# Kernel optimization log

Measured on AMD Instinct MI355X. Metric: run time of the kernel, lower is better.

## Reference

```python
import jax, jax.numpy as jnp
import numpy as np

V = 100000      # num nodes
E = 600000      # num edges (even: first half in-edges, second half out-edges)
D_IN = 128
D_OUT = 128
NREL2 = 100     # num_rel * 2
BN_EPS = 1e-5


def ccorr(a, b):
    # circular correlation along last dim: irfft(conj(rfft(a)) * rfft(b), n=d)
    d = a.shape[-1]
    return jnp.fft.irfft(jnp.conj(jnp.fft.rfft(a)) * jnp.fft.rfft(b), n=d).astype(a.dtype)


def setup_inputs() -> dict:
    key = jax.random.key(0)
    ks = jax.random.split(key, 12)
    return {
        "x": jax.random.normal(ks[0], (V, D_IN), dtype=jnp.float32),
        "rel_repr": jax.random.normal(ks[1], (NREL2, D_IN), dtype=jnp.float32),
        "edge_norm": jax.random.uniform(ks[2], (E,), dtype=jnp.float32),
        "in_w": jax.random.normal(ks[3], (D_IN, D_OUT), dtype=jnp.float32) * 0.05,
        "out_w": jax.random.normal(ks[4], (D_IN, D_OUT), dtype=jnp.float32) * 0.05,
        "loop_w": jax.random.normal(ks[5], (D_IN, D_OUT), dtype=jnp.float32) * 0.05,
        "w_rel": jax.random.normal(ks[6], (D_IN, D_OUT), dtype=jnp.float32) * 0.05,
        "loop_rel": jax.random.normal(ks[7], (1, D_IN), dtype=jnp.float32),
        "bias": jnp.zeros((D_OUT,), dtype=jnp.float32),
        "bn_gamma": jnp.ones((D_OUT,), dtype=jnp.float32),
        "bn_beta": jnp.zeros((D_OUT,), dtype=jnp.float32),
        "edge_src": jax.random.randint(ks[8], (E,), 0, V, dtype=jnp.int32),
        "edge_dst": jax.random.randint(ks[9], (E,), 0, V, dtype=jnp.int32),
        "edge_type": jax.random.randint(ks[10], (E,), 0, NREL2, dtype=jnp.int32),
    }


def reference(x, rel_repr, edge_norm, in_w, out_w, loop_w, w_rel, loop_rel,
              bias, bn_gamma, bn_beta, edge_src, edge_dst, edge_type):
    rel = rel_repr  # rel_wt is None (num_base=-1)
    # gather src features per edge and compose with relation embedding (corr)
    edge_data = ccorr(x[edge_src], rel[edge_type])             # [E, D_IN]
    half = edge_data.shape[0] // 2
    msg = jnp.concatenate(
        [edge_data[:half] @ in_w, edge_data[half:] @ out_w], axis=0
    ) * edge_norm[:, None]                                     # [E, D_OUT]
    # scatter-sum into destination nodes
    agg = jax.ops.segment_sum(msg, edge_dst, num_segments=V)   # [V, D_OUT]
    # self-loop term
    loop = ccorr(x, jnp.broadcast_to(loop_rel, x.shape)) @ loop_w
    h = (agg + loop) / 3.0 + bias
    # BatchNorm1d (training mode: batch stats, biased variance)
    mean = h.mean(axis=0)
    var = h.var(axis=0)
    h = (h - mean) * jax.lax.rsqrt(var + BN_EPS) * bn_gamma + bn_beta
    # act is identity; ltr=True -> project relations
    return h, rel @ w_rel
```

## Files before the change

kernel.cpp:

```cpp
#include <hip/hip_runtime.h>
#include <hip/hip_bf16.h>

#define D 128
constexpr int V_N    = 100000;
constexpr int E_N    = 600000;
constexpr int HALF_E = E_N / 2;
constexpr int NREL2  = 100;
constexpr int NBUCK  = 2 * NREL2;
constexpr float BN_EPS_F = 1e-5f;

constexpr int CHUNK  = 4096;
constexpr int NCHUNK = (E_N + CHUNK - 1) / CHUNK;

typedef short bf16x8  __attribute__((ext_vector_type(8)));
typedef float f32x16  __attribute__((ext_vector_type(16)));
typedef float f32x4v  __attribute__((ext_vector_type(4)));
typedef unsigned int uint32;

constexpr int LOOP_GRID2 = 782;
constexpr size_t MT_BYTES  = 201ull * D * D * 2;
constexpr size_t AGG_BYTES = (size_t)V_N * D * 2;

constexpr size_t P_SS_OFF  = MT_BYTES;
constexpr size_t P_SD_OFF  = P_SS_OFF + (size_t)E_N * 4;
constexpr size_t P_SN_OFF  = P_SD_OFF + (size_t)E_N * 4;
constexpr size_t P_AGG_OFF = P_SN_OFF + (size_t)E_N * 4;
constexpr size_t P_HIST_OFF = P_AGG_OFF;
constexpr size_t P_COFF_OFF = P_HIST_OFF + (size_t)NBUCK * NCHUNK * 4;
constexpr size_t P_CS_OFF  = P_AGG_OFF + AGG_BYTES;
constexpr size_t P_CQ_OFF  = P_CS_OFF + 512;
constexpr size_t P_CNT_OFF = P_CQ_OFF + 512;
constexpr size_t P_ST_OFF  = P_CNT_OFF + 1024;
constexpr size_t WS_NEED_PK = P_ST_OFF + 1024;
constexpr size_t P2_XBF  = (WS_NEED_PK + 255) & ~(size_t)255;
constexpr size_t P2_PSUM = P2_XBF + AGG_BYTES;
constexpr size_t P2_PSQ  = P2_PSUM + 128ull * LOOP_GRID2 * 4;
constexpr size_t WS_NEED2 = P2_PSQ + 128ull * LOOP_GRID2 * 4;

constexpr size_t V4_SS   = MT_BYTES;
constexpr size_t V4_SD   = V4_SS + (size_t)E_N * 4;
constexpr size_t V4_SN   = V4_SD + (size_t)E_N * 4;
constexpr size_t V4_XBF  = V4_SN + (size_t)E_N * 4;
constexpr size_t V4_AGG  = V4_XBF + AGG_BYTES;
constexpr size_t V4_DEG  = V4_AGG + AGG_BYTES;
constexpr size_t V4_CS   = V4_DEG + (size_t)V_N * 4;
constexpr size_t V4_CQ   = V4_CS + 512;
constexpr size_t V4_RP   = V4_CQ + 512;
constexpr size_t V4_CUR  = V4_RP + (size_t)(V_N + 16) * 4;
constexpr size_t V4_EIDX = V4_CUR + (size_t)V_N * 4;
constexpr size_t V4_HIST = V4_EIDX + (size_t)E_N * 4;
constexpr size_t V4_COFF = V4_HIST + (size_t)NBUCK * NCHUNK * 4;
constexpr size_t V4_CNT  = V4_COFF + (size_t)NBUCK * NCHUNK * 4;
constexpr size_t V4_ST   = V4_CNT + 1024;
constexpr size_t V4_BSUM = V4_ST + 1024;
constexpr size_t V4_PSUM = (V4_BSUM + 1024 + 255) & ~(size_t)255;
constexpr size_t V4_PSQ  = V4_PSUM + 128ull * LOOP_GRID2 * 4;
constexpr size_t V4_MSG  = (V4_PSQ + 128ull * LOOP_GRID2 * 4 + 255) & ~(size_t)255;
constexpr size_t WS_NEED4 = V4_MSG + (size_t)E_N * D * 2;

constexpr int SCAN_ELEMS = 1024;
constexpr int NSCANB = (V_N + SCAN_ELEMS - 1) / SCAN_ELEMS;

__device__ inline unsigned short f2bf(float f) {
    __hip_bfloat16 h = __float2bfloat16(f);
    return __builtin_bit_cast(unsigned short, h);
}
__device__ inline float bf2f(unsigned int u) {
    return __uint_as_float(u << 16);
}
__device__ inline int bucket_of(int e, const int* __restrict__ etype) {
    return etype[e] + (e < HALF_E ? 0 : NREL2);
}

__global__ __launch_bounds__(256) void k_hist_chunk(const int* __restrict__ etype,
                                                    int* __restrict__ hist) {
    __shared__ int h[NBUCK];
    for (int i = threadIdx.x; i < NBUCK; i += 256) h[i] = 0;
    __syncthreads();
    int c = blockIdx.x;
    int e0 = c * CHUNK;
#pragma unroll
    for (int r = 0; r < CHUNK / 256; r++) {
        int e = e0 + r * 256 + threadIdx.x;
        if (e < E_N) atomicAdd(&h[bucket_of(e, etype)], 1);
    }
    __syncthreads();
    for (int b = threadIdx.x; b < NBUCK; b += 256) hist[b * NCHUNK + c] = h[b];
}

__global__ void k_scan_bucket(const int* __restrict__ hist, int* __restrict__ chunkoff,
                              int* __restrict__ counts) {
    int b = blockIdx.x, lane = threadIdx.x;
    int acc = 0;
    for (int base = 0; base < NCHUNK; base += 64) {
        int c = base + lane;
        int v = (c < NCHUNK) ? hist[b * NCHUNK + c] : 0;
        int s = v;
#pragma unroll
        for (int off = 1; off < 64; off <<= 1) {
            int t = __shfl(s, lane - off, 64);
            if (lane >= off) s += t;
        }
        if (c < NCHUNK) chunkoff[b * NCHUNK + c] = acc + (s - v);
        acc += __shfl(s, 63, 64);
    }
    if (lane == 0) counts[b] = acc;
}

__global__ void k_scan(const int* __restrict__ counts, int* __restrict__ starts) {
    __shared__ int s[256];
    int i = threadIdx.x;
    int v = (i < NBUCK) ? counts[i] : 0;
    s[i] = v;
    __syncthreads();
    for (int off = 1; off < 256; off <<= 1) {
        int t = (i >= off) ? s[i - off] : 0;
        __syncthreads();
        s[i] += t;
        __syncthreads();
    }
    if (i < NBUCK) starts[i] = s[i] - v;
    if (i == 255) starts[NBUCK] = s[255];
}

__global__ __launch_bounds__(256) void k_scatter2(
    const int* __restrict__ src, const int* __restrict__ dst,
    const float* __restrict__ norm, const int* __restrict__ etype,
    const int* __restrict__ starts, const int* __restrict__ chunkoff,
    int* __restrict__ ssrc, int* __restrict__ sdst, float* __restrict__ snorm) {
    __shared__ int h[NBUCK];
    __shared__ int sbase[NBUCK];
    int c = blockIdx.x;
    for (int b = threadIdx.x; b < NBUCK; b += 256) {
        h[b] = 0;
        sbase[b] = starts[b] + chunkoff[b * NCHUNK + c];
    }
    __syncthreads();
    int e0 = c * CHUNK;
#pragma unroll
    for (int r = 0; r < CHUNK / 256; r++) {
        int e = e0 + r * 256 + threadIdx.x;
        if (e < E_N) {
            int b = bucket_of(e, etype);
            int rank = atomicAdd(&h[b], 1);
            int p = sbase[b] + rank;
            ssrc[p] = src[e]; sdst[p] = dst[e]; snorm[p] = norm[e];
        }
    }
}

constexpr int SETUP_XBF_BLOCKS = 800;
constexpr int SETUP_GRID = 201 + 50 + SETUP_XBF_BLOCKS;
__global__ void k_setup(const float* __restrict__ x, const float* __restrict__ rel,
                        const float* __restrict__ in_w, const float* __restrict__ out_w,
                        const float* __restrict__ loop_rel, const float* __restrict__ loop_w,
                        const float* __restrict__ w_rel, ushort* __restrict__ MT,
                        ushort* __restrict__ xbf, float* __restrict__ out2) {
    extern __shared__ float smem[];
    int blk = blockIdx.x;
    if (blk < 201) {
        float* sW = smem;
        float* sR = smem + D * D;
        int b = blk;
        const float* r = (b < NREL2) ? rel + (size_t)b * D
                       : (b < NBUCK) ? rel + (size_t)(b - NREL2) * D : loop_rel;
        const float* W = (b < NREL2) ? in_w : (b < NBUCK) ? out_w : loop_w;
        for (int i = threadIdx.x; i < D * D; i += blockDim.x) sW[i] = W[i];
        for (int i = threadIdx.x; i < D; i += blockDim.x) { float v = r[i]; sR[i] = v; sR[i + D] = v; }
        __syncthreads();
        int o  = threadIdx.x & 127;
        int jg = threadIdx.x >> 7;
        ushort* MTb = MT + (size_t)b * (D * D);
        for (int pass = 0; pass < 4; pass++) {
            int jbase = jg * 64 + pass * 16;
            float acc[16];
#pragma unroll
            for (int t = 0; t < 16; t++) acc[t] = 0.f;
            for (int k = 0; k < D; k++) {
                float w = sW[k * D + o];
#pragma unroll
                for (int t = 0; t < 16; t++) acc[t] += sR[jbase + t + k] * w;
            }
#pragma unroll
            for (int t = 0; t < 16; t++) MTb[(size_t)o * D + jbase + t] = f2bf(acc[t]);
        }
    } else if (blk < 251) {
        int rr = (blk - 201) * 2 + (threadIdx.x >> 7);
        int o  = threadIdx.x & 127;
        float acc = 0.f;
        for (int k = 0; k < D; k++) acc += rel[rr * D + k] * w_rel[k * D + o];
        out2[rr * D + o] = acc;
    } else {
        const int N8 = V_N * D / 8;
        for (int i = (blk - 251) * 256 + threadIdx.x; i < N8; i += SETUP_XBF_BLOCKS * 256) {
            f32x4v v0 = *(const f32x4v*)&x[(size_t)i * 8];
            f32x4v v1 = *(const f32x4v*)&x[(size_t)i * 8 + 4];
            union { ushort u[8]; uint4 q; } t;
            t.u[0] = f2bf(v0[0]); t.u[1] = f2bf(v0[1]); t.u[2] = f2bf(v0[2]); t.u[3] = f2bf(v0[3]);
            t.u[4] = f2bf(v1[0]); t.u[5] = f2bf(v1[1]); t.u[6] = f2bf(v1[2]); t.u[7] = f2bf(v1[3]);
            *(uint4*)&xbf[(size_t)i * 8] = t.q;
        }
    }
}

__global__ __launch_bounds__(256) void k_deg(const int* __restrict__ sdst,
                                             int* __restrict__ deg) {
    int p = blockIdx.x * 256 + threadIdx.x;
    if (p < E_N) atomicAdd(&deg[sdst[p]], 1);
}

__global__ __launch_bounds__(256) void k_scan1(const int* __restrict__ deg,
                                               int* __restrict__ rowptr,
                                               int* __restrict__ blocksum) {
    __shared__ int s[256];
    int blk = blockIdx.x, tid = threadIdx.x;
    int base = blk * SCAN_ELEMS + tid * 4;
    int v[4]; int tot = 0;
#pragma unroll
    for (int j = 0; j < 4; j++) { int i = base + j; v[j] = (i < V_N) ? deg[i] : 0; tot += v[j]; }
    s[tid] = tot;
    __syncthreads();
    for (int off = 1; off < 256; off <<= 1) {
        int t = (tid >= off) ? s[tid - off] : 0;
        __syncthreads();
        s[tid] += t;
        __syncthreads();
    }
    int run = s[tid] - tot;
#pragma unroll
    for (int j = 0; j < 4; j++) { int i = base + j; if (i < V_N) rowptr[i] = run; run += v[j]; }
    if (tid == 255) blocksum[blk] = s[255];
}

__global__ void k_scan2(int* __restrict__ blocksum) {
    __shared__ int s[128];
    int i = threadIdx.x;
    int v = (i < NSCANB) ? blocksum[i] : 0;
    s[i] = v;
    __syncthreads();
    for (int off = 1; off < 128; off <<= 1) {
        int t = (i >= off) ? s[i - off] : 0;
        __syncthreads();
        s[i] += t;
        __syncthreads();
    }
    if (i < NSCANB) blocksum[i] = s[i] - v;
}

__global__ __launch_bounds__(256) void k_scan3(int* __restrict__ rowptr,
                                               const int* __restrict__ blocksum,
                                               int* __restrict__ cursor) {
    int i = blockIdx.x * 256 + threadIdx.x;
    if (i < V_N) {
        int r = rowptr[i] + blocksum[i >> 10];
        rowptr[i] = r; cursor[i] = r;
    }
    if (i == 0) rowptr[V_N] = E_N;
}

__global__ __launch_bounds__(256) void k_perm(const int* __restrict__ sdst,
                                              int* __restrict__ cursor,
                                              int* __restrict__ eidx) {
    int p = blockIdx.x * 256 + threadIdx.x;
    if (p < E_N) {
        int slot = atomicAdd(&cursor[sdst[p]], 1);
        eidx[slot] = p;
    }
}

constexpr int BPB = 8;

__global__ __launch_bounds__(256) void k_edge_st(
    const ushort* __restrict__ xbf, const ushort* __restrict__ MT,
    const int* __restrict__ starts, const int* __restrict__ ssrc,
    const float* __restrict__ snorm, uint32* __restrict__ msg32) {
    int wid  = threadIdx.x >> 6, lane = threadIdx.x & 63;
    int l31  = lane & 31, l5 = lane >> 5;
    int bucket = blockIdx.x / BPB;
    int sib    = (blockIdx.x % BPB) * 2 + (wid >> 1);
    int oh     = wid & 1;
    int bstart = starts[bucket], bend = starts[bucket + 1];
    const ushort* MTb = MT + (size_t)bucket * (D * D);
    int c0 = oh * 64 + 2 * l31;
    bf16x8 B0[8], B1[8];
#pragma unroll
    for (int kc = 0; kc < 8; kc++) {
        B0[kc] = *(const bf16x8*)&MTb[(size_t)c0 * D + kc * 16 + l5 * 8];
        B1[kc] = *(const bf16x8*)&MTb[(size_t)(c0 + 1) * D + kc * 16 + l5 * 8];
    }
    for (int tbase = bstart + sib * 32; tbase < bend; tbase += BPB * 2 * 32) {
        int nv = bend - tbase; if (nv > 32) nv = 32;
        int sr = ssrc[tbase + (l31 < nv ? l31 : 0)];
        const ushort* xr = xbf + (size_t)sr * D + l5 * 8;
        bf16x8 A[8];
#pragma unroll
        for (int kc = 0; kc < 8; kc++) A[kc] = *(const bf16x8*)(xr + kc * 16);
        f32x16 C0, C1;
#pragma unroll
        for (int i = 0; i < 16; i++) { C0[i] = 0.f; C1[i] = 0.f; }
#pragma unroll
        for (int kc = 0; kc < 8; kc++) {
            C0 = __builtin_amdgcn_mfma_f32_32x32x16_bf16(A[kc], B0[kc], C0, 0, 0, 0);
            C1 = __builtin_amdgcn_mfma_f32_32x32x16_bf16(A[kc], B1[kc], C1, 0, 0, 0);
        }
#pragma unroll
        for (int r = 0; r < 16; r++) {
            int rw = (r & 3) + 8 * (r >> 2) + 4 * l5;
            if (rw < nv) {
                int p = tbase + rw;
                float nm = snorm[p];
                uint32 u = (uint32)f2bf(C0[r] * nm) | ((uint32)f2bf(C1[r] * nm) << 16);
                msg32[(size_t)p * 64 + oh * 32 + l31] = u;
            }
        }
    }
}

__global__ __launch_bounds__(256) void k_segsum(
    const uint32* __restrict__ msg32, const int* __restrict__ eidx,
    const int* __restrict__ rowptr, uint32* __restrict__ agg32) {
    int v = blockIdx.x * 4 + (threadIdx.x >> 6);
    if (v >= V_N) return;
    int lane = threadIdx.x & 63;
    int s = rowptr[v], e = rowptr[v + 1];
    float a0 = 0.f, a1 = 0.f;
    for (int i = s; i < e; i++) {
        int p = eidx[i];
        uint32 u = msg32[(size_t)p * 64 + lane];
        a0 += bf2f(u & 0xffffu); a1 += bf2f(u >> 16);
    }
    agg32[(size_t)v * 64 + lane] = (uint32)f2bf(a0) | ((uint32)f2bf(a1) << 16);
}

__global__ __launch_bounds__(256) void k_loop_pair(
    const ushort* __restrict__ xbf, const ushort* __restrict__ MT,
    const float* __restrict__ bias, const uint32* __restrict__ agg32,
    float* __restrict__ out, float* __restrict__ psum, float* __restrict__ psq) {
    __shared__ float lsum[128], lsq[128];
    if (threadIdx.x < 128) { lsum[threadIdx.x] = 0.f; lsq[threadIdx.x] = 0.f; }
    int wid = threadIdx.x >> 6, lane = threadIdx.x & 63;
    int l31 = lane & 31, l5 = lane >> 5;
    int oh  = wid & 1;
    int strm = blockIdx.x * 2 + (wid >> 1);
    const int NSTR = LOOP_GRID2 * 2;
    const ushort* MTb = MT + (size_t)NBUCK * (D * D);
    int c0 = oh * 64 + 2 * l31;
    int jj = oh * 32 + l31;
    bf16x8 B0[8], B1[8];
#pragma unroll
    for (int kc = 0; kc < 8; kc++) {
        B0[kc] = *(const bf16x8*)&MTb[(size_t)c0 * D + kc * 16 + l5 * 8];
        B1[kc] = *(const bf16x8*)&MTb[(size_t)(c0 + 1) * D + kc * 16 + l5 * 8];
    }
    float b0 = bias[c0], b1 = bias[c0 + 1];
    float ps0 = 0.f, pq0 = 0.f, ps1 = 0.f, pq1 = 0.f;
    const int NT = V_N / 32;
    for (int tile = strm; tile < NT; tile += NSTR) {
        int tbase = tile * 32;
        const ushort* xr = xbf + (size_t)(tbase + l31) * D + l5 * 8;
        bf16x8 A[8];
#pragma unroll
        for (int kc = 0; kc < 8; kc++) A[kc] = *(const bf16x8*)(xr + kc * 16);
        f32x16 C0, C1;
#pragma unroll
        for (int i = 0; i < 16; i++) { C0[i] = 0.f; C1[i] = 0.f; }
#pragma unroll
        for (int kc = 0; kc < 8; kc++) {
            C0 = __builtin_amdgcn_mfma_f32_32x32x16_bf16(A[kc], B0[kc], C0, 0, 0, 0);
            C1 = __builtin_amdgcn_mfma_f32_32x32x16_bf16(A[kc], B1[kc], C1, 0, 0, 0);
        }
#pragma unroll
        for (int r = 0; r < 16; r++) {
            int rw = (r & 3) + 8 * (r >> 2) + 4 * l5;
            int row = tbase + rw;
            uint32 u = agg32[(size_t)row * 64 + jj];
            float h0 = (bf2f(u & 0xffffu) + C0[r]) * (1.f / 3.f) + b0;
            float h1 = (bf2f(u >> 16)     + C1[r]) * (1.f / 3.f) + b1;
            float2 hv = make_float2(h0, h1);
            *(float2*)&out[(size_t)row * D + c0] = hv;
            ps0 += h0; pq0 += h0 * h0;
            ps1 += h1; pq1 += h1 * h1;
        }
    }
    __syncthreads();
    atomicAdd(&lsum[c0], ps0); atomicAdd(&lsq[c0], pq0);
    atomicAdd(&lsum[c0 + 1], ps1); atomicAdd(&lsq[c0 + 1], pq1);
    __syncthreads();
    if (threadIdx.x < 128) {
        psum[(size_t)threadIdx.x * LOOP_GRID2 + blockIdx.x] = lsum[threadIdx.x];
        psq [(size_t)threadIdx.x * LOOP_GRID2 + blockIdx.x] = lsq [threadIdx.x];
    }
}

__global__ __launch_bounds__(256) void k_colreduce(
    const float* __restrict__ psum, const float* __restrict__ psq,
    float* __restrict__ colsum, float* __restrict__ colsq) {
    __shared__ float ls[256], lq[256];
    int c = blockIdx.x, tid = threadIdx.x;
    float s = 0.f, q = 0.f;
    for (int b = tid; b < LOOP_GRID2; b += 256) {
        s += psum[(size_t)c * LOOP_GRID2 + b];
        q += psq [(size_t)c * LOOP_GRID2 + b];
    }
    ls[tid] = s; lq[tid] = q;
    __syncthreads();
    for (int off = 128; off > 0; off >>= 1) {
        if (tid < off) { ls[tid] += ls[tid + off]; lq[tid] += lq[tid + off]; }
        __syncthreads();
    }
    if (tid == 0) { colsum[c] = ls[0]; colsq[c] = lq[0]; }
}

__global__ __launch_bounds__(256) void k_edge_pkb(
    const ushort* __restrict__ xbf, const ushort* __restrict__ MT,
    const int* __restrict__ starts, const int* __restrict__ ssrc,
    const int* __restrict__ sdst, const float* __restrict__ snorm,
    ushort* __restrict__ agg) {
    int wid  = threadIdx.x >> 6, lane = threadIdx.x & 63;
    int l31  = lane & 31, l5 = lane >> 5;
    int bucket = blockIdx.x / BPB;
    int sib    = (blockIdx.x % BPB) * 2 + (wid >> 1);
    int oh     = wid & 1;
    int bstart = starts[bucket], bend = starts[bucket + 1];
    const ushort* MTb = MT + (size_t)bucket * (D * D);
    int c0 = oh * 64 + 2 * l31;
    bf16x8 B0[8], B1[8];
#pragma unroll
    for (int kc = 0; kc < 8; kc++) {
        B0[kc] = *(const bf16x8*)&MTb[(size_t)c0 * D + kc * 16 + l5 * 8];
        B1[kc] = *(const bf16x8*)&MTb[(size_t)(c0 + 1) * D + kc * 16 + l5 * 8];
    }
    for (int tbase = bstart + sib * 32; tbase < bend; tbase += BPB * 2 * 32) {
        int nv = bend - tbase; if (nv > 32) nv = 32;
        int sr = ssrc[tbase + (l31 < nv ? l31 : 0)];
        const ushort* xr = xbf + (size_t)sr * D + l5 * 8;
        bf16x8 A[8];
#pragma unroll
        for (int kc = 0; kc < 8; kc++) A[kc] = *(const bf16x8*)(xr + kc * 16);
        f32x16 C0, C1;
#pragma unroll
        for (int i = 0; i < 16; i++) { C0[i] = 0.f; C1[i] = 0.f; }
#pragma unroll
        for (int kc = 0; kc < 8; kc++) {
            C0 = __builtin_amdgcn_mfma_f32_32x32x16_bf16(A[kc], B0[kc], C0, 0, 0, 0);
            C1 = __builtin_amdgcn_mfma_f32_32x32x16_bf16(A[kc], B1[kc], C1, 0, 0, 0);
        }
#pragma unroll
        for (int r = 0; r < 16; r++) {
            int rw = (r & 3) + 8 * (r >> 2) + 4 * l5;
            if (rw < nv) {
                float nm = snorm[tbase + rw];
                int   dv = sdst[tbase + rw];
                union { ushort u[2]; unsigned int w; } p;
                p.u[0] = f2bf(C0[r] * nm);
                p.u[1] = f2bf(C1[r] * nm);
                ushort* ap = agg + (size_t)dv * D + c0;
                asm volatile("global_atomic_pk_add_bf16 %0, %1, off"
                             :: "v"(ap), "v"(p.w) : "memory");
            }
        }
    }
}

__global__ void k_bn(float* __restrict__ out, const float* __restrict__ colsum,
                     const float* __restrict__ colsq, const float* __restrict__ gamma,
                     const float* __restrict__ beta) {
    const size_t N4 = (size_t)V_N * D / 4;
    size_t stride = (size_t)gridDim.x * blockDim.x;
    for (size_t q = (size_t)blockIdx.x * blockDim.x + threadIdx.x; q < N4; q += stride) {
        int c4 = (int)(q & 31);
        float4 s  = *(const float4*)&colsum[c4 * 4];
        float4 sq = *(const float4*)&colsq[c4 * 4];
        float4 g  = *(const float4*)&gamma[c4 * 4];
        float4 be = *(const float4*)&beta[c4 * 4];
        float4 h  = *(float4*)&out[q * 4];
        const float inv = 1.f / (float)V_N;
        float m0 = s.x * inv, m1 = s.y * inv, m2 = s.z * inv, m3 = s.w * inv;
        float r0 = rsqrtf(sq.x * inv - m0 * m0 + BN_EPS_F);
        float r1 = rsqrtf(sq.y * inv - m1 * m1 + BN_EPS_F);
        float r2 = rsqrtf(sq.z * inv - m2 * m2 + BN_EPS_F);
        float r3 = rsqrtf(sq.w * inv - m3 * m3 + BN_EPS_F);
        h.x = (h.x - m0) * r0 * g.x + be.x;
        h.y = (h.y - m1) * r1 * g.y + be.y;
        h.z = (h.z - m2) * r2 * g.z + be.z;
        h.w = (h.w - m3) * r3 * g.w + be.w;
        *(float4*)&out[q * 4] = h;
    }
}

extern "C" void kernel_launch(void* const* d_in, const int* in_sizes, int n_in,
                              void* d_out, int out_size, void* d_ws, size_t ws_size,
                              hipStream_t stream) {
    const float* x        = (const float*)d_in[0];
    const float* rel      = (const float*)d_in[1];
    const float* enorm    = (const float*)d_in[2];
    const float* in_w     = (const float*)d_in[3];
    const float* out_w    = (const float*)d_in[4];
    const float* loop_w   = (const float*)d_in[5];
    const float* w_rel    = (const float*)d_in[6];
    const float* loop_rel = (const float*)d_in[7];
    const float* bias     = (const float*)d_in[8];
    const float* gamma    = (const float*)d_in[9];
    const float* beta     = (const float*)d_in[10];
    const int*   esrc     = (const int*)d_in[11];
    const int*   edst     = (const int*)d_in[12];
    const int*   etype    = (const int*)d_in[13];
    float* out = (float*)d_out;
    char*  ws  = (char*)d_ws;

    const int smem = (D * D + 256) * sizeof(float);
    const int gE = (E_N + 255) / 256;

    if (ws_size >= WS_NEED4) {
        ushort* MT     = (ushort*)(ws + 0);
        int*    ssrc   = (int*)(ws + V4_SS);
        int*    sdst   = (int*)(ws + V4_SD);
        float*  snorm  = (float*)(ws + V4_SN);
        ushort* xbf    = (ushort*)(ws + V4_XBF);
        uint32* agg32  = (uint32*)(ws + V4_AGG);
        int*    deg    = (int*)(ws + V4_DEG);
        float*  colsum = (float*)(ws + V4_CS);
        float*  colsq  = (float*)(ws + V4_CQ);
        int*    rowptr = (int*)(ws + V4_RP);
        int*    cursor = (int*)(ws + V4_CUR);
        int*    eidx   = (int*)(ws + V4_EIDX);
        int*    hist   = (int*)(ws + V4_HIST);
        int*    coff   = (int*)(ws + V4_COFF);
        int*    counts = (int*)(ws + V4_CNT);
        int*    starts = (int*)(ws + V4_ST);
        int*    bsum   = (int*)(ws + V4_BSUM);
        float*  psum   = (float*)(ws + V4_PSUM);
        float*  psq    = (float*)(ws + V4_PSQ);
        uint32* msg32  = (uint32*)(ws + V4_MSG);

        hipMemsetAsync(ws + V4_DEG, 0, (size_t)V_N * 4, stream);

        k_hist_chunk<<<NCHUNK, 256, 0, stream>>>(etype, hist);
        k_scan_bucket<<<NBUCK, 64, 0, stream>>>(hist, coff, counts);
        k_scan<<<1, 256, 0, stream>>>(counts, starts);
        k_scatter2<<<NCHUNK, 256, 0, stream>>>(esrc, edst, enorm, etype, starts, coff,
                                               ssrc, sdst, snorm);
        k_setup<<<SETUP_GRID, 256, smem, stream>>>(x, rel, in_w, out_w, loop_rel, loop_w,
                                                   w_rel, MT, xbf, out + (size_t)V_N * D);
        k_deg<<<gE, 256, 0, stream>>>(sdst, deg);
        k_scan1<<<NSCANB, 256, 0, stream>>>(deg, rowptr, bsum);
        k_scan2<<<1, 128, 0, stream>>>(bsum);
        k_scan3<<<(V_N + 255) / 256, 256, 0, stream>>>(rowptr, bsum, cursor);
        k_perm<<<gE, 256, 0, stream>>>(sdst, cursor, eidx);

        k_edge_st<<<NBUCK * BPB, 256, 0, stream>>>(xbf, MT, starts, ssrc, snorm, msg32);
        k_segsum<<<(V_N + 3) / 4, 256, 0, stream>>>(msg32, eidx, rowptr, agg32);

        k_loop_pair<<<LOOP_GRID2, 256, 0, stream>>>(xbf, MT, bias, agg32, out, psum, psq);
        k_colreduce<<<128, 256, 0, stream>>>(psum, psq, colsum, colsq);
        k_bn<<<2048, 256, 0, stream>>>(out, colsum, colsq, gamma, beta);
    } else {
        ushort* MT     = (ushort*)(ws + 0);
        int*    ssrc   = (int*)(ws + P_SS_OFF);
        int*    sdst   = (int*)(ws + P_SD_OFF);
        float*  snorm  = (float*)(ws + P_SN_OFF);
        ushort* aggbf  = (ushort*)(ws + P_AGG_OFF);
        uint32* agg32  = (uint32*)(ws + P_AGG_OFF);
        int*    hist   = (int*)(ws + P_HIST_OFF);
        int*    coff   = (int*)(ws + P_COFF_OFF);
        float*  colsum = (float*)(ws + P_CS_OFF);
        float*  colsq  = (float*)(ws + P_CQ_OFF);
        int*    counts = (int*)(ws + P_CNT_OFF);
        int*    starts = (int*)(ws + P_ST_OFF);
        ushort* xbf    = (ushort*)(ws + P2_XBF);
        float*  psum   = (float*)(ws + P2_PSUM);
        float*  psq    = (float*)(ws + P2_PSQ);

        k_hist_chunk<<<NCHUNK, 256, 0, stream>>>(etype, hist);
        k_scan_bucket<<<NBUCK, 64, 0, stream>>>(hist, coff, counts);
        k_scan<<<1, 256, 0, stream>>>(counts, starts);
        k_scatter2<<<NCHUNK, 256, 0, stream>>>(esrc, edst, enorm, etype, starts, coff,
                                               ssrc, sdst, snorm);
        hipMemsetAsync(ws + P_AGG_OFF, 0, AGG_BYTES, stream);
        k_setup<<<SETUP_GRID, 256, smem, stream>>>(x, rel, in_w, out_w, loop_rel, loop_w,
                                                   w_rel, MT, xbf, out + (size_t)V_N * D);
        k_edge_pkb<<<NBUCK * BPB, 256, 0, stream>>>(xbf, MT, starts, ssrc, sdst, snorm, aggbf);
        k_loop_pair<<<LOOP_GRID2, 256, 0, stream>>>(xbf, MT, bias, agg32, out, psum, psq);
        k_colreduce<<<128, 256, 0, stream>>>(psum, psq, colsum, colsq);
        k_bn<<<2048, 256, 0, stream>>>(out, colsum, colsq, gamma, beta);
    }
}
```

Baseline: 507.2 us.

## Fuse segment-sum into self-loop GEMM and degree count into edge scatter

Removes the separate segment-sum kernel and its bf16 aggregate buffer by gathering each node's messages directly in the self-loop MFMA kernel's epilogue, which now uses a larger grid. Degree counting moves into the bucket scatter kernel, removing a separate launch and a re-read of the sorted destinations. The edge message kernel gets more blocks per bucket. The fused epilogue runs per-row CSR loops of varying length inside an MFMA wave, which can cause divergence and less regular memory access than the dedicated segment-sum kernel.

```diff
diff --git a/kernel.cpp b/kernel.cpp
--- a/kernel.cpp
+++ b/kernel.cpp
@@ -17,10 +17,10 @@
 typedef float f32x4v  __attribute__((ext_vector_type(4)));
 typedef unsigned int uint32;
 
-constexpr int LOOP_GRID2 = 782;
 constexpr size_t MT_BYTES  = 201ull * D * D * 2;
 constexpr size_t AGG_BYTES = (size_t)V_N * D * 2;
 
+constexpr int LOOP_GRID2 = 782;
 constexpr size_t P_SS_OFF  = MT_BYTES;
 constexpr size_t P_SD_OFF  = P_SS_OFF + (size_t)E_N * 4;
 constexpr size_t P_SN_OFF  = P_SD_OFF + (size_t)E_N * 4;
@@ -37,26 +37,26 @@
 constexpr size_t P2_PSQ  = P2_PSUM + 128ull * LOOP_GRID2 * 4;
 constexpr size_t WS_NEED2 = P2_PSQ + 128ull * LOOP_GRID2 * 4;
 
-constexpr size_t V4_SS   = MT_BYTES;
-constexpr size_t V4_SD   = V4_SS + (size_t)E_N * 4;
-constexpr size_t V4_SN   = V4_SD + (size_t)E_N * 4;
-constexpr size_t V4_XBF  = V4_SN + (size_t)E_N * 4;
-constexpr size_t V4_AGG  = V4_XBF + AGG_BYTES;
-constexpr size_t V4_DEG  = V4_AGG + AGG_BYTES;
-constexpr size_t V4_CS   = V4_DEG + (size_t)V_N * 4;
-constexpr size_t V4_CQ   = V4_CS + 512;
-constexpr size_t V4_RP   = V4_CQ + 512;
-constexpr size_t V4_CUR  = V4_RP + (size_t)(V_N + 16) * 4;
-constexpr size_t V4_EIDX = V4_CUR + (size_t)V_N * 4;
-constexpr size_t V4_HIST = V4_EIDX + (size_t)E_N * 4;
-constexpr size_t V4_COFF = V4_HIST + (size_t)NBUCK * NCHUNK * 4;
-constexpr size_t V4_CNT  = V4_COFF + (size_t)NBUCK * NCHUNK * 4;
-constexpr size_t V4_ST   = V4_CNT + 1024;
-constexpr size_t V4_BSUM = V4_ST + 1024;
-constexpr size_t V4_PSUM = (V4_BSUM + 1024 + 255) & ~(size_t)255;
-constexpr size_t V4_PSQ  = V4_PSUM + 128ull * LOOP_GRID2 * 4;
-constexpr size_t V4_MSG  = (V4_PSQ + 128ull * LOOP_GRID2 * 4 + 255) & ~(size_t)255;
-constexpr size_t WS_NEED4 = V4_MSG + (size_t)E_N * D * 2;
+constexpr int LOOP_GRID3 = 1563;
+constexpr size_t V5_SS   = MT_BYTES;
+constexpr size_t V5_SD   = V5_SS + (size_t)E_N * 4;
+constexpr size_t V5_SN   = V5_SD + (size_t)E_N * 4;
+constexpr size_t V5_XBF  = V5_SN + (size_t)E_N * 4;
+constexpr size_t V5_DEG  = V5_XBF + AGG_BYTES;
+constexpr size_t V5_CS   = V5_DEG + (size_t)V_N * 4;
+constexpr size_t V5_CQ   = V5_CS + 512;
+constexpr size_t V5_RP   = V5_CQ + 512;
+constexpr size_t V5_CUR  = V5_RP + (size_t)(V_N + 16) * 4;
+constexpr size_t V5_EIDX = V5_CUR + (size_t)V_N * 4;
+constexpr size_t V5_HIST = V5_EIDX + (size_t)E_N * 4;
+constexpr size_t V5_COFF = V5_HIST + (size_t)NBUCK * NCHUNK * 4;
+constexpr size_t V5_CNT  = V5_COFF + (size_t)NBUCK * NCHUNK * 4;
+constexpr size_t V5_ST   = V5_CNT + 1024;
+constexpr size_t V5_BSUM = V5_ST + 1024;
+constexpr size_t V5_PSUM = (V5_BSUM + 1024 + 255) & ~(size_t)255;
+constexpr size_t V5_PSQ  = V5_PSUM + 128ull * LOOP_GRID3 * 4;
+constexpr size_t V5_MSG  = (V5_PSQ + 128ull * LOOP_GRID3 * 4 + 255) & ~(size_t)255;
+constexpr size_t WS_NEED5 = V5_MSG + (size_t)E_N * D * 2;
 
 constexpr int SCAN_ELEMS = 1024;
 constexpr int NSCANB = (V_N + SCAN_ELEMS - 1) / SCAN_ELEMS;
@@ -123,11 +123,12 @@
     if (i == 255) starts[NBUCK] = s[255];
 }
 
-__global__ __launch_bounds__(256) void k_scatter2(
+__global__ __launch_bounds__(256) void k_scatter3(
     const int* __restrict__ src, const int* __restrict__ dst,
     const float* __restrict__ norm, const int* __restrict__ etype,
     const int* __restrict__ starts, const int* __restrict__ chunkoff,
-    int* __restrict__ ssrc, int* __restrict__ sdst, float* __restrict__ snorm) {
+    int* __restrict__ ssrc, int* __restrict__ sdst, float* __restrict__ snorm,
+    int* __restrict__ deg) {
     __shared__ int h[NBUCK];
     __shared__ int sbase[NBUCK];
     int c = blockIdx.x;
@@ -142,9 +143,11 @@
         int e = e0 + r * 256 + threadIdx.x;
         if (e < E_N) {
             int b = bucket_of(e, etype);
+            int dv = dst[e];
             int rank = atomicAdd(&h[b], 1);
             int p = sbase[b] + rank;
-            ssrc[p] = src[e]; sdst[p] = dst[e]; snorm[p] = norm[e];
+            ssrc[p] = src[e]; sdst[p] = dv; snorm[p] = norm[e];
+            atomicAdd(&deg[dv], 1);
         }
     }
 }
@@ -203,12 +206,6 @@
     }
 }
 
-__global__ __launch_bounds__(256) void k_deg(const int* __restrict__ sdst,
-                                             int* __restrict__ deg) {
-    int p = blockIdx.x * 256 + threadIdx.x;
-    if (p < E_N) atomicAdd(&deg[sdst[p]], 1);
-}
-
 __global__ __launch_bounds__(256) void k_scan1(const int* __restrict__ deg,
                                                int* __restrict__ rowptr,
                                                int* __restrict__ blocksum) {
@@ -268,12 +265,170 @@
     }
 }
 
-constexpr int BPB = 8;
-
+constexpr int EBPB = 16;
 __global__ __launch_bounds__(256) void k_edge_st(
     const ushort* __restrict__ xbf, const ushort* __restrict__ MT,
     const int* __restrict__ starts, const int* __restrict__ ssrc,
     const float* __restrict__ snorm, uint32* __restrict__ msg32) {
+    int wid  = threadIdx.x >> 6, lane = threadIdx.x & 63;
+    int l31  = lane & 31, l5 = lane >> 5;
+    int bucket = blockIdx.x / EBPB;
+    int sib    = (blockIdx.x % EBPB) * 2 + (wid >> 1);
+    int oh     = wid & 1;
+    int bstart = starts[bucket], bend = starts[bucket + 1];
+    const ushort* MTb = MT + (size_t)bucket * (D * D);
+    int c0 = oh * 64 + 2 * l31;
+    bf16x8 B0[8], B1[8];
+#pragma unroll
+    for (int kc = 0; kc < 8; kc++) {
+        B0[kc] = *(const bf16x8*)&MTb[(size_t)c0 * D + kc * 16 + l5 * 8];
+        B1[kc] = *(const bf16x8*)&MTb[(size_t)(c0 + 1) * D + kc * 16 + l5 * 8];
+    }
+    for (int tbase = bstart + sib * 32; tbase < bend; tbase += EBPB * 2 * 32) {
+        int nv = bend - tbase; if (nv > 32) nv = 32;
+        int sr = ssrc[tbase + (l31 < nv ? l31 : 0)];
+        const ushort* xr = xbf + (size_t)sr * D + l5 * 8;
+        bf16x8 A[8];
+#pragma unroll
+        for (int kc = 0; kc < 8; kc++) A[kc] = *(const bf16x8*)(xr + kc * 16);
+        f32x16 C0, C1;
+#pragma unroll
+        for (int i = 0; i < 16; i++) { C0[i] = 0.f; C1[i] = 0.f; }
+#pragma unroll
+        for (int kc = 0; kc < 8; kc++) {
+            C0 = __builtin_amdgcn_mfma_f32_32x32x16_bf16(A[kc], B0[kc], C0, 0, 0, 0);
+            C1 = __builtin_amdgcn_mfma_f32_32x32x16_bf16(A[kc], B1[kc], C1, 0, 0, 0);
+        }
+#pragma unroll
+        for (int r = 0; r < 16; r++) {
+            int rw = (r & 3) + 8 * (r >> 2) + 4 * l5;
+            if (rw < nv) {
+                int p = tbase + rw;
+                float nm = snorm[p];
+                uint32 u = (uint32)f2bf(C0[r] * nm) | ((uint32)f2bf(C1[r] * nm) << 16);
+                msg32[(size_t)p * 64 + oh * 32 + l31] = u;
+            }
+        }
+    }
+}
+
+__global__ __launch_bounds__(256) void k_loop_fused(
+    const ushort* __restrict__ xbf, const ushort* __restrict__ MT,
+    const float* __restrict__ bias, const uint32* __restrict__ msg32,
+    const int* __restrict__ eidx, const int* __restrict__ rowptr,
+    float* __restrict__ out, float* __restrict__ psum, float* __restrict__ psq) {
+    __shared__ float lsum[128], lsq[128];
+    if (threadIdx.x < 128) { lsum[threadIdx.x] = 0.f; lsq[threadIdx.x] = 0.f; }
+    int wid = threadIdx.x >> 6, lane = threadIdx.x & 63;
+    int l31 = lane & 31, l5 = lane >> 5;
+    int oh  = wid & 1;
+    int strm = blockIdx.x * 2 + (wid >> 1);
+    const int NSTR = LOOP_GRID3 * 2;
+    const ushort* MTb = MT + (size_t)NBUCK * (D * D);
+    int c0 = oh * 64 + 2 * l31;
+    int jj = oh * 32 + l31;
+    bf16x8 B0[8], B1[8];
+#pragma unroll
+    for (int kc = 0; kc < 8; kc++) {
+        B0[kc] = *(const bf16x8*)&MTb[(size_t)c0 * D + kc * 16 + l5 * 8];
+        B1[kc] = *(const bf16x8*)&MTb[(size_t)(c0 + 1) * D + kc * 16 + l5 * 8];
+    }
+    float b0 = bias[c0], b1 = bias[c0 + 1];
+    float ps0 = 0.f, pq0 = 0.f, ps1 = 0.f, pq1 = 0.f;
+    const int NT = V_N / 32;
+    for (int tile = strm; tile < NT; tile += NSTR) {
+        int tbase = tile * 32;
+        const ushort* xr = xbf + (size_t)(tbase + l31) * D + l5 * 8;
+        bf16x8 A[8];
+#pragma unroll
+        for (int kc = 0; kc < 8; kc++) A[kc] = *(const bf16x8*)(xr + kc * 16);
+        f32x16 C0, C1;
+#pragma unroll
+        for (int i = 0; i < 16; i++) { C0[i] = 0.f; C1[i] = 0.f; }
+#pragma unroll
+        for (int kc = 0; kc < 8; kc++) {
+            C0 = __builtin_amdgcn_mfma_f32_32x32x16_bf16(A[kc], B0[kc], C0, 0, 0, 0);
+            C1 = __builtin_amdgcn_mfma_f32_32x32x16_bf16(A[kc], B1[kc], C1, 0, 0, 0);
+        }
+#pragma unroll
+        for (int r = 0; r < 16; r++) {
+            int rw = (r & 3) + 8 * (r >> 2) + 4 * l5;
+            int row = tbase + rw;
+            int s = rowptr[row], e = rowptr[row + 1];
+            float a0 = 0.f, a1 = 0.f;
+            for (int i = s; i < e; i++) {
+                int p = eidx[i];
+                uint32 u = msg32[(size_t)p * 64 + jj];
+                a0 += bf2f(u & 0xffffu); a1 += bf2f(u >> 16);
+            }
+            float h0 = (a0 + C0[r]) * (1.f / 3.f) + b0;
+            float h1 = (a1 + C1[r]) * (1.f / 3.f) + b1;
+            *(float2*)&out[(size_t)row * D + c0] = make_float2(h0, h1);
+            ps0 += h0; pq0 += h0 * h0;
+            ps1 += h1; pq1 += h1 * h1;
+        }
+    }
+    __syncthreads();
+    atomicAdd(&lsum[c0], ps0); atomicAdd(&lsq[c0], pq0);
+    atomicAdd(&lsum[c0 + 1], ps1); atomicAdd(&lsq[c0 + 1], pq1);
+    __syncthreads();
+    if (threadIdx.x < 128) {
+        psum[(size_t)threadIdx.x * LOOP_GRID3 + blockIdx.x] = lsum[threadIdx.x];
+        psq [(size_t)threadIdx.x * LOOP_GRID3 + blockIdx.x] = lsq [threadIdx.x];
+    }
+}
+
+__global__ __launch_bounds__(256) void k_colreduce(
+    const float* __restrict__ psum, const float* __restrict__ psq,
+    float* __restrict__ colsum, float* __restrict__ colsq, int nblk) {
+    __shared__ float ls[256], lq[256];
+    int c = blockIdx.x, tid = threadIdx.x;
+    float s = 0.f, q = 0.f;
+    for (int b = tid; b < nblk; b += 256) {
+        s += psum[(size_t)c * nblk + b];
+        q += psq [(size_t)c * nblk + b];
+    }
+    ls[tid] = s; lq[tid] = q;
+    __syncthreads();
+    for (int off = 128; off > 0; off >>= 1) {
+        if (tid < off) { ls[tid] += ls[tid + off]; lq[tid] += lq[tid + off]; }
+        __syncthreads();
+    }
+    if (tid == 0) { colsum[c] = ls[0]; colsq[c] = lq[0]; }
+}
+
+constexpr int BPB = 8;
+__global__ __launch_bounds__(256) void k_scatter2(
+    const int* __restrict__ src, const int* __restrict__ dst,
+    const float* __restrict__ norm, const int* __restrict__ etype,
+    const int* __restrict__ starts, const int* __restrict__ chunkoff,
+    int* __restrict__ ssrc, int* __restrict__ sdst, float* __restrict__ snorm) {
+    __shared__ int h[NBUCK];
+    __shared__ int sbase[NBUCK];
+    int c = blockIdx.x;
+    for (int b = threadIdx.x; b < NBUCK; b += 256) {
+        h[b] = 0;
+        sbase[b] = starts[b] + chunkoff[b * NCHUNK + c];
+    }
+    __syncthreads();
+    int e0 = c * CHUNK;
+#pragma unroll
+    for (int r = 0; r < CHUNK / 256; r++) {
+        int e = e0 + r * 256 + threadIdx.x;
+        if (e < E_N) {
+            int b = bucket_of(e, etype);
+            int rank = atomicAdd(&h[b], 1);
+            int p = sbase[b] + rank;
+            ssrc[p] = src[e]; sdst[p] = dst[e]; snorm[p] = norm[e];
+        }
+    }
+}
+
+__global__ __launch_bounds__(256) void k_edge_pkb(
+    const ushort* __restrict__ xbf, const ushort* __restrict__ MT,
+    const int* __restrict__ starts, const int* __restrict__ ssrc,
+    const int* __restrict__ sdst, const float* __restrict__ snorm,
+    ushort* __restrict__ agg) {
     int wid  = threadIdx.x >> 6, lane = threadIdx.x & 63;
     int l31  = lane & 31, l5 = lane >> 5;
     int bucket = blockIdx.x / BPB;
@@ -307,29 +462,17 @@
         for (int r = 0; r < 16; r++) {
             int rw = (r & 3) + 8 * (r >> 2) + 4 * l5;
             if (rw < nv) {
-                int p = tbase + rw;
-                float nm = snorm[p];
-                uint32 u = (uint32)f2bf(C0[r] * nm) | ((uint32)f2bf(C1[r] * nm) << 16);
-                msg32[(size_t)p * 64 + oh * 32 + l31] = u;
+                float nm = snorm[tbase + rw];
+                int   dv = sdst[tbase + rw];
+                union { ushort u[2]; unsigned int w; } p;
+                p.u[0] = f2bf(C0[r] * nm);
+                p.u[1] = f2bf(C1[r] * nm);
+                ushort* ap = agg + (size_t)dv * D + c0;
+                asm volatile("global_atomic_pk_add_bf16 %0, %1, off"
+                             :: "v"(ap), "v"(p.w) : "memory");
             }
         }
     }
-}
-
-__global__ __launch_bounds__(256) void k_segsum(
-    const uint32* __restrict__ msg32, const int* __restrict__ eidx,
-    const int* __restrict__ rowptr, uint32* __restrict__ agg32) {
-    int v = blockIdx.x * 4 + (threadIdx.x >> 6);
-    if (v >= V_N) return;
-    int lane = threadIdx.x & 63;
-    int s = rowptr[v], e = rowptr[v + 1];
-    float a0 = 0.f, a1 = 0.f;
-    for (int i = s; i < e; i++) {
-        int p = eidx[i];
-        uint32 u = msg32[(size_t)p * 64 + lane];
-        a0 += bf2f(u & 0xffffu); a1 += bf2f(u >> 16);
-    }
-    agg32[(size_t)v * 64 + lane] = (uint32)f2bf(a0) | ((uint32)f2bf(a1) << 16);
 }
 
 __global__ __launch_bounds__(256) void k_loop_pair(
@@ -376,8 +519,7 @@
             uint32 u = agg32[(size_t)row * 64 + jj];
             float h0 = (bf2f(u & 0xffffu) + C0[r]) * (1.f / 3.f) + b0;
             float h1 = (bf2f(u >> 16)     + C1[r]) * (1.f / 3.f) + b1;
-            float2 hv = make_float2(h0, h1);
-            *(float2*)&out[(size_t)row * D + c0] = hv;
+            *(float2*)&out[(size_t)row * D + c0] = make_float2(h0, h1);
             ps0 += h0; pq0 += h0 * h0;
             ps1 += h1; pq1 += h1 * h1;
         }
@@ -389,76 +531,6 @@
     if (threadIdx.x < 128) {
         psum[(size_t)threadIdx.x * LOOP_GRID2 + blockIdx.x] = lsum[threadIdx.x];
         psq [(size_t)threadIdx.x * LOOP_GRID2 + blockIdx.x] = lsq [threadIdx.x];
-    }
-}
-
-__global__ __launch_bounds__(256) void k_colreduce(
-    const float* __restrict__ psum, const float* __restrict__ psq,
-    float* __restrict__ colsum, float* __restrict__ colsq) {
-    __shared__ float ls[256], lq[256];
-    int c = blockIdx.x, tid = threadIdx.x;
-    float s = 0.f, q = 0.f;
-    for (int b = tid; b < LOOP_GRID2; b += 256) {
-        s += psum[(size_t)c * LOOP_GRID2 + b];
-        q += psq [(size_t)c * LOOP_GRID2 + b];
-    }
-    ls[tid] = s; lq[tid] = q;
-    __syncthreads();
-    for (int off = 128; off > 0; off >>= 1) {
-        if (tid < off) { ls[tid] += ls[tid + off]; lq[tid] += lq[tid + off]; }
-        __syncthreads();
-    }
-    if (tid == 0) { colsum[c] = ls[0]; colsq[c] = lq[0]; }
-}
-
-__global__ __launch_bounds__(256) void k_edge_pkb(
-    const ushort* __restrict__ xbf, const ushort* __restrict__ MT,
-    const int* __restrict__ starts, const int* __restrict__ ssrc,
-    const int* __restrict__ sdst, const float* __restrict__ snorm,
-    ushort* __restrict__ agg) {
-    int wid  = threadIdx.x >> 6, lane = threadIdx.x & 63;
-    int l31  = lane & 31, l5 = lane >> 5;
-    int bucket = blockIdx.x / BPB;
-    int sib    = (blockIdx.x % BPB) * 2 + (wid >> 1);
-    int oh     = wid & 1;
-    int bstart = starts[bucket], bend = starts[bucket + 1];
-    const ushort* MTb = MT + (size_t)bucket * (D * D);
-    int c0 = oh * 64 + 2 * l31;
-    bf16x8 B0[8], B1[8];
-#pragma unroll
-    for (int kc = 0; kc < 8; kc++) {
-        B0[kc] = *(const bf16x8*)&MTb[(size_t)c0 * D + kc * 16 + l5 * 8];
-        B1[kc] = *(const bf16x8*)&MTb[(size_t)(c0 + 1) * D + kc * 16 + l5 * 8];
-    }
-    for (int tbase = bstart + sib * 32; tbase < bend; tbase += BPB * 2 * 32) {
-        int nv = bend - tbase; if (nv > 32) nv = 32;
-        int sr = ssrc[tbase + (l31 < nv ? l31 : 0)];
-        const ushort* xr = xbf + (size_t)sr * D + l5 * 8;
-        bf16x8 A[8];
-#pragma unroll
-        for (int kc = 0; kc < 8; kc++) A[kc] = *(const bf16x8*)(xr + kc * 16);
-        f32x16 C0, C1;
-#pragma unroll
-        for (int i = 0; i < 16; i++) { C0[i] = 0.f; C1[i] = 0.f; }
-#pragma unroll
-        for (int kc = 0; kc < 8; kc++) {
-            C0 = __builtin_amdgcn_mfma_f32_32x32x16_bf16(A[kc], B0[kc], C0, 0, 0, 0);
-            C1 = __builtin_amdgcn_mfma_f32_32x32x16_bf16(A[kc], B1[kc], C1, 0, 0, 0);
-        }
-#pragma unroll
-        for (int r = 0; r < 16; r++) {
-            int rw = (r & 3) + 8 * (r >> 2) + 4 * l5;
-            if (rw < nv) {
-                float nm = snorm[tbase + rw];
-                int   dv = sdst[tbase + rw];
-                union { ushort u[2]; unsigned int w; } p;
-                p.u[0] = f2bf(C0[r] * nm);
-                p.u[1] = f2bf(C1[r] * nm);
-                ushort* ap = agg + (size_t)dv * D + c0;
-                asm volatile("global_atomic_pk_add_bf16 %0, %1, off"
-                             :: "v"(ap), "v"(p.w) : "memory");
-            }
-        }
     }
 }
 
@@ -511,48 +583,45 @@
     const int smem = (D * D + 256) * sizeof(float);
     const int gE = (E_N + 255) / 256;
 
-    if (ws_size >= WS_NEED4) {
+    if (ws_size >= WS_NEED5) {
         ushort* MT     = (ushort*)(ws + 0);
-        int*    ssrc   = (int*)(ws + V4_SS);
-        int*    sdst   = (int*)(ws + V4_SD);
-        float*  snorm  = (float*)(ws + V4_SN);
-        ushort* xbf    = (ushort*)(ws + V4_XBF);
-        uint32* agg32  = (uint32*)(ws + V4_AGG);
-        int*    deg    = (int*)(ws + V4_DEG);
-        float*  colsum = (float*)(ws + V4_CS);
-        float*  colsq  = (float*)(ws + V4_CQ);
-        int*    rowptr = (int*)(ws + V4_RP);
-        int*    cursor = (int*)(ws + V4_CUR);
-        int*    eidx   = (int*)(ws + V4_EIDX);
-        int*    hist   = (int*)(ws + V4_HIST);
-        int*    coff   = (int*)(ws + V4_COFF);
-        int*    counts = (int*)(ws + V4_CNT);
-        int*    starts = (int*)(ws + V4_ST);
-        int*    bsum   = (int*)(ws + V4_BSUM);
-        float*  psum   = (float*)(ws + V4_PSUM);
-        float*  psq    = (float*)(ws + V4_PSQ);
-        uint32* msg32  = (uint32*)(ws + V4_MSG);
-
-        hipMemsetAsync(ws + V4_DEG, 0, (size_t)V_N * 4, stream);
+        int*    ssrc   = (int*)(ws + V5_SS);
+        int*    sdst   = (int*)(ws + V5_SD);
+        float*  snorm  = (float*)(ws + V5_SN);
+        ushort* xbf    = (ushort*)(ws + V5_XBF);
+        int*    deg    = (int*)(ws + V5_DEG);
+        float*  colsum = (float*)(ws + V5_CS);
+        float*  colsq  = (float*)(ws + V5_CQ);
+        int*    rowptr = (int*)(ws + V5_RP);
+        int*    cursor = (int*)(ws + V5_CUR);
+        int*    eidx   = (int*)(ws + V5_EIDX);
+        int*    hist   = (int*)(ws + V5_HIST);
+        int*    coff   = (int*)(ws + V5_COFF);
+        int*    counts = (int*)(ws + V5_CNT);
+        int*    starts = (int*)(ws + V5_ST);
+        int*    bsum   = (int*)(ws + V5_BSUM);
+        float*  psum   = (float*)(ws + V5_PSUM);
+        float*  psq    = (float*)(ws + V5_PSQ);
+        uint32* msg32  = (uint32*)(ws + V5_MSG);
+
+        hipMemsetAsync(ws + V5_DEG, 0, (size_t)V_N * 4, stream);
 
         k_hist_chunk<<<NCHUNK, 256, 0, stream>>>(etype, hist);
         k_scan_bucket<<<NBUCK, 64, 0, stream>>>(hist, coff, counts);
         k_scan<<<1, 256, 0, stream>>>(counts, starts);
-        k_scatter2<<<NCHUNK, 256, 0, stream>>>(esrc, edst, enorm, etype, starts, coff,
-                                               ssrc, sdst, snorm);
+        k_scatter3<<<NCHUNK, 256, 0, stream>>>(esrc, edst, enorm, etype, starts, coff,
+                                               ssrc, sdst, snorm, deg);
         k_setup<<<SETUP_GRID, 256, smem, stream>>>(x, rel, in_w, out_w, loop_rel, loop_w,
                                                    w_rel, MT, xbf, out + (size_t)V_N * D);
-        k_deg<<<gE, 256, 0, stream>>>(sdst, deg);
         k_scan1<<<NSCANB, 256, 0, stream>>>(deg, rowptr, bsum);
         k_scan2<<<1, 128, 0, stream>>>(bsum);
         k_scan3<<<(V_N + 255) / 256, 256, 0, stream>>>(rowptr, bsum, cursor);
         k_perm<<<gE, 256, 0, stream>>>(sdst, cursor, eidx);
 
-        k_edge_st<<<NBUCK * BPB, 256, 0, stream>>>(xbf, MT, starts, ssrc, snorm, msg32);
-        k_segsum<<<(V_N + 3) / 4, 256, 0, stream>>>(msg32, eidx, rowptr, agg32);
-
-        k_loop_pair<<<LOOP_GRID2, 256, 0, stream>>>(xbf, MT, bias, agg32, out, psum, psq);
-        k_colreduce<<<128, 256, 0, stream>>>(psum, psq, colsum, colsq);
+        k_edge_st<<<NBUCK * EBPB, 256, 0, stream>>>(xbf, MT, starts, ssrc, snorm, msg32);
+        k_loop_fused<<<LOOP_GRID3, 256, 0, stream>>>(xbf, MT, bias, msg32, eidx, rowptr,
+                                                     out, psum, psq);
+        k_colreduce<<<128, 256, 0, stream>>>(psum, psq, colsum, colsq, LOOP_GRID3);
         k_bn<<<2048, 256, 0, stream>>>(out, colsum, colsq, gamma, beta);
     } else {
         ushort* MT     = (ushort*)(ws + 0);
@@ -581,7 +650,7 @@
                                                    w_rel, MT, xbf, out + (size_t)V_N * D);
         k_edge_pkb<<<NBUCK * BPB, 256, 0, stream>>>(xbf, MT, starts, ssrc, sdst, snorm, aggbf);
         k_loop_pair<<<LOOP_GRID2, 256, 0, stream>>>(xbf, MT, bias, agg32, out, psum, psq);
-        k_colreduce<<<128, 256, 0, stream>>>(psum, psq, colsum, colsq);
+        k_colreduce<<<128, 256, 0, stream>>>(psum, psq, colsum, colsq, LOOP_GRID2);
         k_bn<<<2048, 256, 0, stream>>>(out, colsum, colsq, gamma, beta);
     }
 }
```

Result: slower. 606.6 us (+19.6%).
